# Kernel tuning notes

Measured on AMD Instinct MI355X. Metric: run time of the kernel, lower is better.

The kernel has to match this reference:

```python
import jax, jax.numpy as jnp
import numpy as np

N_EXPERTS = 16
TOP_K = 4
N_GROUP = 4
TOPK_GROUP = 2
NORM_TOPK = True
ROUTED_SCALE = 2.5
H = 2048
F_MOE = 1024
F_SHARED = 2048
B, S = 2, 2048


def setup_inputs() -> dict:
    key = jax.random.key(0)
    ks = jax.random.split(key, 9)
    std = 0.02
    return {
        "hidden_states": jax.random.normal(ks[0], (B, S, H), jnp.float32),
        "gate_weight": jax.random.normal(ks[1], (N_EXPERTS, H), jnp.float32) * std,
        "e_score_correction_bias": jnp.zeros((N_EXPERTS,), jnp.float32),
        "gate_w": jax.random.normal(ks[2], (N_EXPERTS, F_MOE, H), jnp.float32) * std,
        "up_w": jax.random.normal(ks[3], (N_EXPERTS, F_MOE, H), jnp.float32) * std,
        "down_w": jax.random.normal(ks[4], (N_EXPERTS, H, F_MOE), jnp.float32) * std,
        "sh_gate_w": jax.random.normal(ks[5], (F_SHARED, H), jnp.float32) * std,
        "sh_up_w": jax.random.normal(ks[6], (F_SHARED, H), jnp.float32) * std,
        "sh_down_w": jax.random.normal(ks[7], (H, F_SHARED), jnp.float32) * std,
    }


def _route(hidden, gate_weight, bias):
    # hidden: [T, H] -> topk_weight [T, K], topk_idx [T, K]
    T = hidden.shape[0]
    epg = N_EXPERTS // N_GROUP
    logits = hidden @ gate_weight.T                     # [T, N]
    scores = jax.nn.sigmoid(logits)
    scores_for_choice = scores + bias[None, :]
    # group score = sum of top-2 per group
    grp = scores_for_choice.reshape(T, N_GROUP, epg)
    group_scores = jax.lax.top_k(grp, 2)[0].sum(-1)      # [T, G]
    group_idx = jax.lax.top_k(group_scores, TOPK_GROUP)[1]
    group_mask = jax.nn.one_hot(group_idx, N_GROUP, dtype=jnp.bool_).any(1)  # [T, G]
    score_mask = jnp.repeat(group_mask, epg, axis=-1)    # [T, N]
    masked = jnp.where(score_mask, scores_for_choice, -jnp.inf)
    topk_idx = jax.lax.top_k(masked, TOP_K)[1]           # [T, K]
    topk_weight = jnp.take_along_axis(scores, topk_idx, axis=1)  # raw sigmoid scores
    return topk_weight, topk_idx


def _swiglu(x, gw, uw, dw):
    return (jax.nn.silu(x @ gw.T) * (x @ uw.T)) @ dw.T


def reference(hidden_states, gate_weight, e_score_correction_bias,
              gate_w, up_w, down_w, sh_gate_w, sh_up_w, sh_down_w):
    Bh, Sh, Hh = hidden_states.shape
    hidden = hidden_states.reshape(-1, Hh)               # [T, H]
    topk_weight, topk_idx = _route(hidden, gate_weight, e_score_correction_bias)
    if NORM_TOPK:
        topk_weight = topk_weight / (topk_weight.sum(-1, keepdims=True) + 1e-20)
    topk_weight = topk_weight * ROUTED_SCALE
    # dense dispatch weight matrix [T, N] (sum of one-hot * weight over k)
    one_hot = jax.nn.one_hot(topk_idx, N_EXPERTS, dtype=topk_weight.dtype)
    weight_matrix = (one_hot * topk_weight[..., None]).sum(1)
    # run all experts densely (faithful to original)
    g = jnp.einsum('th,nfh->ntf', hidden, gate_w)        # [N, T, F]
    u = jnp.einsum('th,nfh->ntf', hidden, up_w)
    act = jax.nn.silu(g) * u
    routed = jnp.einsum('ntf,nhf,tn->th', act, down_w, weight_matrix)
    out = routed + _swiglu(hidden, sh_gate_w, sh_up_w, sh_down_w)
    return out.reshape(Bh, Sh, Hh)
```

## Files before the change

### kernel.cpp

```cpp
#include <hip/hip_runtime.h>
#include <cstdint>

typedef unsigned int u32;
typedef unsigned short u16;
typedef __bf16 bf16x8 __attribute__((ext_vector_type(8)));
typedef float f32x4 __attribute__((ext_vector_type(4)));

#define NTOK 4096
#define HDIM 2048
#define FMOE 1024
#define FSH  2048
#define NEXP 16

__device__ __forceinline__ u16 f2bf(float f) {
  u32 u = __float_as_uint(f);
  u32 r = (u + 0x7fffu + ((u >> 16) & 1u)) >> 16;
  return (u16)r;
}
__device__ __forceinline__ float bf2f(u16 h) {
  return __uint_as_float(((u32)h) << 16);
}

__device__ __forceinline__ void gld_lds16(const void* g, void* l) {
  __builtin_amdgcn_global_load_lds(
      (const __attribute__((address_space(1))) u32*)g,
      (__attribute__((address_space(3))) u32*)l, 16, 0, 0);
}

__global__ void cvt_bf16(const float* __restrict__ in, u16* __restrict__ out, long n4) {
  long i = (long)blockIdx.x * blockDim.x + threadIdx.x;
  if (i < n4) {
    float4 v = ((const float4*)in)[i];
    ushort4 o;
    o.x = f2bf(v.x); o.y = f2bf(v.y); o.z = f2bf(v.z); o.w = f2bf(v.w);
    ((ushort4*)out)[i] = o;
  }
}

__global__ void cvt_pair_moe(const float* __restrict__ g, const float* __restrict__ u,
                             u16* __restrict__ dst) {
  int e = blockIdx.z;
  const long n4 = (long)FMOE * HDIM / 4;
  long i = (long)blockIdx.x * blockDim.x + threadIdx.x;
  const float4* gs = (const float4*)(g + (long)e * FMOE * HDIM);
  const float4* us = (const float4*)(u + (long)e * FMOE * HDIM);
  ushort4* d = (ushort4*)(dst + (long)e * 2 * FMOE * HDIM);
  float4 v = gs[i];
  ushort4 o;
  o.x = f2bf(v.x); o.y = f2bf(v.y); o.z = f2bf(v.z); o.w = f2bf(v.w);
  d[i] = o;
  v = us[i];
  o.x = f2bf(v.x); o.y = f2bf(v.y); o.z = f2bf(v.z); o.w = f2bf(v.w);
  d[n4 + i] = o;
}

__global__ __launch_bounds__(256) void routing_kernel(
    const float* __restrict__ hidden, const float* __restrict__ gw,
    const float* __restrict__ bias, int* __restrict__ topk_idx,
    float* __restrict__ topk_w) {
  __shared__ float gws[8 * HDIM];
  int tid = threadIdx.x, lane = tid & 63, wv = tid >> 6;
  int t = blockIdx.x * 4 + wv;
  float acc[NEXP];
#pragma unroll
  for (int n = 0; n < NEXP; ++n) acc[n] = 0.f;
  const float4* h4 = (const float4*)(hidden + (long)t * HDIM);

  for (int half = 0; half < 2; ++half) {
    for (int i = tid; i < 8 * HDIM / 4; i += 256)
      ((float4*)gws)[i] = ((const float4*)(gw + half * 8 * HDIM))[i];
    __syncthreads();
#pragma unroll
    for (int j0 = 0; j0 < HDIM / 4; j0 += 64) {
      int j = j0 + lane;
      float4 hv = h4[j];
#pragma unroll
      for (int e = 0; e < 8; ++e) {
        float4 g = ((const float4*)gws)[e * (HDIM / 4) + j];
        acc[half * 8 + e] += hv.x * g.x + hv.y * g.y + hv.z * g.z + hv.w * g.w;
      }
    }
    __syncthreads();
  }
#pragma unroll
  for (int n = 0; n < NEXP; ++n) {
    float v = acc[n];
    for (int m = 32; m; m >>= 1) v += __shfl_xor(v, m);
    acc[n] = v;
  }
  if (lane == 0) {
    float sc[NEXP], scb[NEXP];
#pragma unroll
    for (int n = 0; n < NEXP; ++n) {
      sc[n] = 1.f / (1.f + expf(-acc[n]));
      scb[n] = sc[n] + bias[n];
    }
    float gs[4];
#pragma unroll
    for (int g = 0; g < 4; ++g) {
      float m1 = -1e30f, m2 = -1e30f;
#pragma unroll
      for (int j = 0; j < 4; ++j) {
        float v = scb[4 * g + j];
        if (v > m1) { m2 = m1; m1 = v; } else if (v > m2) { m2 = v; }
      }
      gs[g] = m1 + m2;
    }
    int g1 = -1, g2 = -1;
    { float b = -1e30f; for (int g = 0; g < 4; ++g) if (gs[g] > b) { b = gs[g]; g1 = g; } }
    { float b = -1e30f; for (int g = 0; g < 4; ++g) if (g != g1 && gs[g] > b) { b = gs[g]; g2 = g; } }
    bool used[NEXP];
#pragma unroll
    for (int n = 0; n < NEXP; ++n) used[n] = false;
    int sel[4]; float wts[4]; float s = 0.f;
    for (int k = 0; k < 4; ++k) {
      float b = -1e30f; int bi = 0;
      for (int n = 0; n < NEXP; ++n) {
        int g = n >> 2;
        if ((g == g1 || g == g2) && !used[n] && scb[n] > b) { b = scb[n]; bi = n; }
      }
      used[bi] = true; sel[k] = bi; wts[k] = sc[bi]; s += sc[bi];
    }
    float inv = 2.5f / (s + 1e-20f);
    for (int k = 0; k < 4; ++k) {
      topk_idx[t * 4 + k] = sel[k];
      topk_w[t * 4 + k] = wts[k] * inv;
    }
  }
}

__global__ __launch_bounds__(256) void count_prefix(const int* __restrict__ topki,
                                                    int* __restrict__ offs) {
  __shared__ int wsum[4][NEXP];
  int tid = threadIdx.x, lane = tid & 63, wv = tid >> 6;
  int c[NEXP];
#pragma unroll
  for (int e = 0; e < NEXP; ++e) c[e] = 0;
  for (int i0 = wv * 64; i0 < NTOK * 4; i0 += 256) {
    int v = topki[i0 + lane];
#pragma unroll
    for (int e = 0; e < NEXP; ++e) {
      unsigned long long b = __ballot(v == e);
      if (lane == 0) c[e] += __popcll(b);
    }
  }
  if (lane == 0) {
#pragma unroll
    for (int e = 0; e < NEXP; ++e) wsum[wv][e] = c[e];
  }
  __syncthreads();
  if (tid == 0) {
    int s = 0;
    for (int e = 0; e < NEXP; ++e) {
      int t = wsum[0][e] + wsum[1][e] + wsum[2][e] + wsum[3][e];
      offs[e] = s;
      s += t;
    }
    offs[NEXP] = s;
  }
}

__global__ void fill_lists(const int* __restrict__ topk_idx,
                           const int* __restrict__ offs, int* __restrict__ ltok,
                           int* __restrict__ slotmap) {
  int e = blockIdx.x;
  int tid = threadIdx.x, lane = tid & 63, wv = tid >> 6;
  __shared__ int cursor;
  __shared__ int wcnt[4];
  if (tid == 0) cursor = offs[e];
  __syncthreads();
  for (int base = 0; base < NTOK; base += 256) {
    int t = base + tid;
    int flag = 0, kk = 0;
#pragma unroll
    for (int k = 0; k < 4; ++k) {
      if (topk_idx[t * 4 + k] == e) { flag = 1; kk = k; }
    }
    unsigned long long b = __ballot(flag);
    if (lane == 0) wcnt[wv] = __popcll(b);
    __syncthreads();
    int pre = 0;
    for (int i = 0; i < wv; ++i) pre += wcnt[i];
    int pos = cursor + pre + __popcll(b & ((1ull << lane) - 1ull));
    if (flag) { ltok[pos] = t; slotmap[t * 4 + kk] = pos; }
    __syncthreads();
    if (tid == 0) cursor += wcnt[0] + wcnt[1] + wcnt[2] + wcnt[3];
    __syncthreads();
  }
}

template <int F>
__global__ void silu_mul_pair(u16* __restrict__ gu, const int* __restrict__ nrows_ptr,
                              int nrows_static) {
  int rows = nrows_ptr ? *nrows_ptr : nrows_static;
  long total4 = (long)rows * (F / 4);
  long i = (long)blockIdx.x * blockDim.x + threadIdx.x;
  if (i < total4) {
    long row = i / (F / 4);
    int f4 = (int)(i - row * (F / 4));
    ushort4* rowp = (ushort4*)(gu + row * 2 * F);
    ushort4 gv = rowp[f4];
    ushort4 uv = rowp[F / 4 + f4];
    float gf, uf, sv;
    ushort4 o;
    gf = bf2f(gv.x); uf = bf2f(uv.x); sv = gf / (1.f + __expf(-gf)); o.x = f2bf(sv * uf);
    gf = bf2f(gv.y); uf = bf2f(uv.y); sv = gf / (1.f + __expf(-gf)); o.y = f2bf(sv * uf);
    gf = bf2f(gv.z); uf = bf2f(uv.z); sv = gf / (1.f + __expf(-gf)); o.z = f2bf(sv * uf);
    gf = bf2f(gv.w); uf = bf2f(uv.w); sv = gf / (1.f + __expf(-gf)); o.w = f2bf(sv * uf);
    rowp[f4] = o;
  }
}

__global__ void reduce_out(const u16* __restrict__ SY, const u16* __restrict__ Y,
                           const int* __restrict__ slotmap, const float* __restrict__ tkw,
                           float* __restrict__ out) {
  long i = (long)blockIdx.x * blockDim.x + threadIdx.x;
  int t = (int)(i >> 9);
  int c4 = (int)(i & 511);
  ushort4 s = ((const ushort4*)SY)[i];
  float4 o;
  o.x = bf2f(s.x); o.y = bf2f(s.y); o.z = bf2f(s.z); o.w = bf2f(s.w);
#pragma unroll
  for (int k = 0; k < 4; ++k) {
    int sl = slotmap[t * 4 + k];
    float w = tkw[t * 4 + k];
    ushort4 y = ((const ushort4*)Y)[(long)sl * 512 + c4];
    o.x += w * bf2f(y.x);
    o.y += w * bf2f(y.y);
    o.z += w * bf2f(y.z);
    o.w += w * bf2f(y.w);
  }
  ((float4*)out)[i] = o;
}

#define LGKM0 asm volatile("s_waitcnt lgkmcnt(0)" ::: "memory")
#define VMC4  asm volatile("s_waitcnt vmcnt(4)" ::: "memory")
#define VMC0  asm volatile("s_waitcnt vmcnt(0)" ::: "memory")
__device__ __forceinline__ void bar() {
  asm volatile("" ::: "memory");
  __builtin_amdgcn_s_barrier();
  asm volatile("" ::: "memory");
}

__global__ __launch_bounds__(512, 2) void gemm256(
    const u16* __restrict__ A, const u16* __restrict__ B, u16* __restrict__ C,
    const int* __restrict__ gather, const int* __restrict__ offs,
    int Mstatic, int N, int K, int lda, long Bstride) {
  int e = blockIdx.z;
  int seg0 = 0, segM = Mstatic;
  if (offs) { seg0 = offs[e]; segM = offs[e + 1] - seg0; }
  int mt = blockIdx.y, nt = blockIdx.x;
  if (mt * 256 >= segM) return;
  const u16* Be = B + (long)e * Bstride;

  __shared__ __align__(16) u16 sm[65536];

  int tid = threadIdx.x;
  int lane = tid & 63;
  int wv = tid >> 6, wm = wv >> 2, wn = wv & 3;
  int c4 = lane & 15, r4 = lane >> 4;

  int srow = tid >> 3, schunk = tid & 7;
  int sswz8 = (schunk ^ (srow & 7)) * 8;
  int sOff = srow * 64 + schunk * 8;

  u32 aoff[2][2], boff[2][2];
#pragma unroll
  for (int h = 0; h < 2; ++h)
#pragma unroll
    for (int j = 0; j < 2; ++j) {
      int rit = h * 128 + j * 64 + srow;
      int rl = mt * 256 + rit;
      if (rl >= segM) rl = mt * 256;
      int ridx = seg0 + rl;
      u32 arow = gather ? (u32)gather[ridx] : (u32)ridx;
      aoff[h][j] = arow * (u32)lda + (u32)sswz8;
      boff[h][j] = (u32)(nt * 256 + rit) * (u32)K + (u32)sswz8;
    }

  int swzv = (lane & 7) * 8;
  int aRL0 = c4 * 64 + ((r4 * 8) ^ swzv);
  int aRL1 = aRL0 ^ 32;
  int aB0 = wm * 8192, aB1 = 32768 + aB0;
  int bB0 = 16384 + wn * 4096, bB1 = 32768 + bB0;

  f32x4 acc[8][4];
  bf16x8 af[4][2], bLo[2][2], bHi[2][2];
#pragma unroll
  for (int i = 0; i < 8; ++i)
#pragma unroll
    for (int j = 0; j < 4; ++j) acc[i][j] = f32x4{0.f, 0.f, 0.f, 0.f};

#define READ_A8(BASE) do { _Pragma("unroll") \
  for (int mi = 0; mi < 4; ++mi) { \
    af[mi][0] = *(const bf16x8*)&sm[(BASE) + mi * 1024 + aRL0]; \
    af[mi][1] = *(const bf16x8*)&sm[(BASE) + mi * 1024 + aRL1]; \
  } } while (0)
#define READ_B4(BASE, BARR) do { _Pragma("unroll") \
  for (int ni = 0; ni < 2; ++ni) { \
    BARR[ni][0] = *(const bf16x8*)&sm[(BASE) + ni * 1024 + aRL0]; \
    BARR[ni][1] = *(const bf16x8*)&sm[(BASE) + ni * 1024 + aRL1]; \
  } } while (0)
#define MFMAQ(MI0, NI0, BARR) do { __builtin_amdgcn_s_setprio(1); \
  _Pragma("unroll") for (int mi = 0; mi < 4; ++mi) \
  _Pragma("unroll") for (int ni = 0; ni < 2; ++ni) \
  _Pragma("unroll") for (int kk = 0; kk < 2; ++kk) \
    acc[(MI0) + mi][(NI0) + ni] = __builtin_amdgcn_mfma_f32_16x16x32_bf16( \
        af[mi][kk], BARR[ni][kk], acc[(MI0) + mi][(NI0) + ni], 0, 0, 0); \
  __builtin_amdgcn_s_setprio(0); } while (0)
#define STAGE_A(PO, H, T) do { \
  gld_lds16(A + aoff[H][0] + (u32)((T) * 64), &sm[(PO) + (H) * 8192 + sOff]); \
  gld_lds16(A + aoff[H][1] + (u32)((T) * 64), &sm[(PO) + (H) * 8192 + 4096 + sOff]); \
} while (0)
#define STAGE_B(PO, H, T) do { \
  gld_lds16(Be + boff[H][0] + (u32)((T) * 64), &sm[(PO) + 16384 + (H) * 8192 + sOff]); \
  gld_lds16(Be + boff[H][1] + (u32)((T) * 64), &sm[(PO) + 16384 + (H) * 8192 + 4096 + sOff]); \
} while (0)

  STAGE_A(0, 0, 0); STAGE_A(0, 1, 0); STAGE_B(0, 0, 0); STAGE_B(0, 1, 0);
  STAGE_B(32768, 0, 1); STAGE_B(32768, 1, 1);
  VMC4;
  bar();

  int niter = K >> 7;
  for (int it = 0; it < niter; ++it) {
    int to = 2 * it + 1, t2 = 2 * it + 2, t3 = 2 * it + 3;
    bool nl = (it + 1 < niter);
    READ_A8(aB0); READ_B4(bB0, bLo);
    STAGE_A(32768, 0, to);
    bar(); LGKM0; MFMAQ(0, 0, bLo); bar();
    READ_B4(bB0 + 2048, bHi);
    STAGE_A(32768, 1, to);
    bar(); LGKM0; MFMAQ(0, 2, bHi); bar();
    READ_A8(aB0 + 4096);
    if (nl) STAGE_B(0, 0, t2);
    bar(); LGKM0; MFMAQ(4, 2, bHi); bar();
    if (nl) { STAGE_B(0, 1, t2); VMC4; } else { VMC0; }
    bar(); MFMAQ(4, 0, bLo); bar();
    READ_A8(aB1); READ_B4(bB1, bLo);
    if (nl) STAGE_A(0, 0, t2);
    bar(); LGKM0; MFMAQ(0, 0, bLo); bar();
    READ_B4(bB1 + 2048, bHi);
    if (nl) STAGE_A(0, 1, t2);
    bar(); LGKM0; MFMAQ(0, 2, bHi); bar();
    READ_A8(aB1 + 4096);
    if (nl) STAGE_B(32768, 0, t3);
    bar(); LGKM0; MFMAQ(4, 2, bHi); bar();
    if (nl) { STAGE_B(32768, 1, t3); VMC4; }
    bar(); MFMAQ(4, 0, bLo); bar();
  }

#undef READ_A8
#undef READ_B4
#undef MFMAQ
#undef STAGE_A
#undef STAGE_B

#pragma unroll
  for (int mi = 0; mi < 8; ++mi) {
#pragma unroll
    for (int r = 0; r < 4; ++r) {
      int lr = wm * 128 + mi * 16 + r4 * 4 + r;
      if (mt * 256 + lr < segM) {
        long base = (long)(seg0 + mt * 256 + lr) * N + nt * 256 + wn * 64 + c4;
#pragma unroll
        for (int ni = 0; ni < 4; ++ni) C[base + ni * 16] = f2bf(acc[mi][ni][r]);
      }
    }
  }
}

extern "C" void kernel_launch(void* const* d_in, const int* in_sizes, int n_in,
                              void* d_out, int out_size, void* d_ws, size_t ws_size,
                              hipStream_t stream) {
  const float* hidden = (const float*)d_in[0];
  const float* gate_weight = (const float*)d_in[1];
  const float* bias = (const float*)d_in[2];
  const float* gate_w = (const float*)d_in[3];
  const float* up_w = (const float*)d_in[4];
  const float* down_w = (const float*)d_in[5];
  const float* shg = (const float*)d_in[6];
  const float* shu = (const float*)d_in[7];
  const float* shd = (const float*)d_in[8];
  float* out = (float*)d_out;

  char* p = (char*)d_ws;
  auto alloc = [&](size_t bytes) {
    char* q = p;
    p += (bytes + 255) & ~(size_t)255;
    return q;
  };
  u16* Xb = (u16*)alloc((size_t)NTOK * HDIM * 2);
  u16* GUb = (u16*)alloc((size_t)NEXP * 2 * FMOE * HDIM * 2);
  u16* Db = (u16*)alloc((size_t)NEXP * HDIM * FMOE * 2);
  u16* SGUb = (u16*)alloc((size_t)2 * FSH * HDIM * 2);
  u16* SDb = (u16*)alloc((size_t)HDIM * FSH * 2);
  u16* gu_out = (u16*)alloc((size_t)NTOK * 4 * 2 * FMOE * 2);
  int* topki = (int*)alloc((size_t)NTOK * 4 * 4);
  float* topkw = (float*)alloc((size_t)NTOK * 4 * 4);
  int* offs = (int*)alloc(128);
  int* ltok = (int*)alloc((size_t)NTOK * 4 * 4);
  int* slotmap = (int*)alloc((size_t)NTOK * 4 * 4);
  u16* Y = GUb;
  u16* gs_out = GUb + (size_t)NTOK * 4 * HDIM;
  u16* SY = gs_out + (size_t)NTOK * 2 * FSH;

  cvt_bf16<<<8192, 256, 0, stream>>>(hidden, Xb, (long)NTOK * HDIM / 4);
  cvt_pair_moe<<<dim3(2048, 1, NEXP), 256, 0, stream>>>(gate_w, up_w, GUb);
  cvt_bf16<<<32768, 256, 0, stream>>>(down_w, Db, (long)NEXP * HDIM * FMOE / 4);
  cvt_bf16<<<4096, 256, 0, stream>>>(shg, SGUb, (long)FSH * HDIM / 4);
  cvt_bf16<<<4096, 256, 0, stream>>>(shu, SGUb + (size_t)FSH * HDIM, (long)FSH * HDIM / 4);
  cvt_bf16<<<4096, 256, 0, stream>>>(shd, SDb, (long)HDIM * FSH / 4);

  routing_kernel<<<NTOK / 4, 256, 0, stream>>>(hidden, gate_weight, bias, topki, topkw);
  count_prefix<<<1, 256, 0, stream>>>(topki, offs);
  fill_lists<<<NEXP, 256, 0, stream>>>(topki, offs, ltok, slotmap);

  gemm256<<<dim3(2 * FMOE / 256, NTOK / 256, NEXP), 512, 0, stream>>>(
      Xb, GUb, gu_out, ltok, offs, 0, 2 * FMOE, HDIM, HDIM, (long)2 * FMOE * HDIM);
  silu_mul_pair<FMOE><<<16384, 256, 0, stream>>>(gu_out, offs + NEXP, 0);
  gemm256<<<dim3(HDIM / 256, NTOK / 256, NEXP), 512, 0, stream>>>(
      gu_out, Db, Y, nullptr, offs, 0, HDIM, FMOE, 2 * FMOE, (long)HDIM * FMOE);

  gemm256<<<dim3(2 * FSH / 256, NTOK / 256, 1), 512, 0, stream>>>(
      Xb, SGUb, gs_out, nullptr, nullptr, NTOK, 2 * FSH, HDIM, HDIM, 0);
  silu_mul_pair<FSH><<<8192, 256, 0, stream>>>(gs_out, nullptr, NTOK);
  gemm256<<<dim3(HDIM / 256, NTOK / 256, 1), 512, 0, stream>>>(
      gs_out, SDb, SY, nullptr, nullptr, NTOK, HDIM, FSH, 2 * FSH, 0);

  reduce_out<<<8192, 256, 0, stream>>>(SY, Y, slotmap, topkw, out);
}
```

Before: 962.8 us.

## Fuse SiLU-mul into gate/up GEMM epilogue via interleaved weight layout

Weights for gate and up projections are reordered during conversion so that each 256-column GEMM tile holds 128 gate and 128 up columns. The GEMM epilogue then exchanges the up half through shared memory and writes silu(g)*u directly, which removes the separate silu_mul kernels and halves the intermediate buffer written and read by the down GEMM. Separately, the routing kernel drops the LDS staging of gate weights and reads them directly from global/cache with the hidden row held in registers. This costs extra LDS traffic and barriers in the epilogue, plus strided scatter writes in the conversion kernel.

```diff
diff --git a/kernel.cpp b/kernel.cpp
--- a/kernel.cpp
+++ b/kernel.cpp
@@ -37,50 +37,50 @@
   }
 }
 
-__global__ void cvt_pair_moe(const float* __restrict__ g, const float* __restrict__ u,
-                             u16* __restrict__ dst) {
+template <int F>
+__global__ void cvt_pair(const float* __restrict__ g, const float* __restrict__ u,
+                         u16* __restrict__ dst) {
   int e = blockIdx.z;
-  const long n4 = (long)FMOE * HDIM / 4;
+  const long n4 = (long)F * HDIM / 4;
   long i = (long)blockIdx.x * blockDim.x + threadIdx.x;
-  const float4* gs = (const float4*)(g + (long)e * FMOE * HDIM);
-  const float4* us = (const float4*)(u + (long)e * FMOE * HDIM);
-  ushort4* d = (ushort4*)(dst + (long)e * 2 * FMOE * HDIM);
+  if (i >= n4) return;
+  int f = (int)(i >> 9);
+  int c = (int)(i & 511);
+  const float4* gs = (const float4*)(g + (long)e * F * HDIM);
+  const float4* us = (const float4*)(u + (long)e * F * HDIM);
+  ushort4* d = (ushort4*)(dst + (long)e * 2 * F * HDIM);
+  long rg = (long)(256 * (f >> 7) + (f & 127)) * 512 + c;
+  long ru = rg + 128 * 512;
   float4 v = gs[i];
   ushort4 o;
   o.x = f2bf(v.x); o.y = f2bf(v.y); o.z = f2bf(v.z); o.w = f2bf(v.w);
-  d[i] = o;
+  d[rg] = o;
   v = us[i];
   o.x = f2bf(v.x); o.y = f2bf(v.y); o.z = f2bf(v.z); o.w = f2bf(v.w);
-  d[n4 + i] = o;
+  d[ru] = o;
 }
 
 __global__ __launch_bounds__(256) void routing_kernel(
     const float* __restrict__ hidden, const float* __restrict__ gw,
     const float* __restrict__ bias, int* __restrict__ topk_idx,
     float* __restrict__ topk_w) {
-  __shared__ float gws[8 * HDIM];
   int tid = threadIdx.x, lane = tid & 63, wv = tid >> 6;
   int t = blockIdx.x * 4 + wv;
+  const float4* h4 = (const float4*)(hidden + (long)t * HDIM);
+  const float4* g4 = (const float4*)gw;
+  float4 hv[8];
+#pragma unroll
+  for (int j = 0; j < 8; ++j) hv[j] = h4[lane + 64 * j];
   float acc[NEXP];
 #pragma unroll
-  for (int n = 0; n < NEXP; ++n) acc[n] = 0.f;
-  const float4* h4 = (const float4*)(hidden + (long)t * HDIM);
-
-  for (int half = 0; half < 2; ++half) {
-    for (int i = tid; i < 8 * HDIM / 4; i += 256)
-      ((float4*)gws)[i] = ((const float4*)(gw + half * 8 * HDIM))[i];
-    __syncthreads();
-#pragma unroll
-    for (int j0 = 0; j0 < HDIM / 4; j0 += 64) {
-      int j = j0 + lane;
-      float4 hv = h4[j];
-#pragma unroll
-      for (int e = 0; e < 8; ++e) {
-        float4 g = ((const float4*)gws)[e * (HDIM / 4) + j];
-        acc[half * 8 + e] += hv.x * g.x + hv.y * g.y + hv.z * g.z + hv.w * g.w;
-      }
-    }
-    __syncthreads();
+  for (int e = 0; e < NEXP; ++e) {
+    float a = 0.f;
+#pragma unroll
+    for (int j = 0; j < 8; ++j) {
+      float4 g = g4[e * 512 + lane + 64 * j];
+      a += hv[j].x * g.x + hv[j].y * g.y + hv[j].z * g.z + hv[j].w * g.w;
+    }
+    acc[e] = a;
   }
 #pragma unroll
   for (int n = 0; n < NEXP; ++n) {
@@ -189,28 +189,6 @@
   }
 }
 
-template <int F>
-__global__ void silu_mul_pair(u16* __restrict__ gu, const int* __restrict__ nrows_ptr,
-                              int nrows_static) {
-  int rows = nrows_ptr ? *nrows_ptr : nrows_static;
-  long total4 = (long)rows * (F / 4);
-  long i = (long)blockIdx.x * blockDim.x + threadIdx.x;
-  if (i < total4) {
-    long row = i / (F / 4);
-    int f4 = (int)(i - row * (F / 4));
-    ushort4* rowp = (ushort4*)(gu + row * 2 * F);
-    ushort4 gv = rowp[f4];
-    ushort4 uv = rowp[F / 4 + f4];
-    float gf, uf, sv;
-    ushort4 o;
-    gf = bf2f(gv.x); uf = bf2f(uv.x); sv = gf / (1.f + __expf(-gf)); o.x = f2bf(sv * uf);
-    gf = bf2f(gv.y); uf = bf2f(uv.y); sv = gf / (1.f + __expf(-gf)); o.y = f2bf(sv * uf);
-    gf = bf2f(gv.z); uf = bf2f(uv.z); sv = gf / (1.f + __expf(-gf)); o.z = f2bf(sv * uf);
-    gf = bf2f(gv.w); uf = bf2f(uv.w); sv = gf / (1.f + __expf(-gf)); o.w = f2bf(sv * uf);
-    rowp[f4] = o;
-  }
-}
-
 __global__ void reduce_out(const u16* __restrict__ SY, const u16* __restrict__ Y,
                            const int* __restrict__ slotmap, const float* __restrict__ tkw,
                            float* __restrict__ out) {
@@ -245,7 +223,7 @@
 __global__ __launch_bounds__(512, 2) void gemm256(
     const u16* __restrict__ A, const u16* __restrict__ B, u16* __restrict__ C,
     const int* __restrict__ gather, const int* __restrict__ offs,
-    int Mstatic, int N, int K, int lda, long Bstride) {
+    int Mstatic, int N, int K, int lda, long Bstride, int fuse) {
   int e = blockIdx.z;
   int seg0 = 0, segM = Mstatic;
   if (offs) { seg0 = offs[e]; segM = offs[e + 1] - seg0; }
@@ -356,15 +334,85 @@
 #undef STAGE_A
 #undef STAGE_B
 
-#pragma unroll
-  for (int mi = 0; mi < 8; ++mi) {
-#pragma unroll
-    for (int r = 0; r < 4; ++r) {
-      int lr = wm * 128 + mi * 16 + r4 * 4 + r;
-      if (mt * 256 + lr < segM) {
-        long base = (long)(seg0 + mt * 256 + lr) * N + nt * 256 + wn * 64 + c4;
-#pragma unroll
-        for (int ni = 0; ni < 4; ++ni) C[base + ni * 16] = f2bf(acc[mi][ni][r]);
+  if (fuse) {
+    if (wn >= 2) {
+#pragma unroll
+      for (int mi = 0; mi < 4; ++mi)
+#pragma unroll
+        for (int ni = 0; ni < 4; ++ni)
+#pragma unroll
+          for (int r = 0; r < 4; ++r) {
+            int rloc = mi * 16 + r4 * 4 + r;
+            int floc = (wn - 2) * 64 + ni * 16 + c4;
+            sm[(wm * 128 + rloc) * 128 + floc] = f2bf(acc[mi + 4 * 0][ni][r]);
+          }
+    }
+    __syncthreads();
+    if (wn < 2) {
+#pragma unroll
+      for (int mi = 0; mi < 4; ++mi)
+#pragma unroll
+        for (int r = 0; r < 4; ++r) {
+          int rloc = mi * 16 + r4 * 4 + r;
+          int lr = wm * 128 + rloc;
+          if (mt * 256 + lr < segM) {
+            long base = (long)(seg0 + mt * 256 + lr) * (N >> 1) + nt * 128 + wn * 64 + c4;
+#pragma unroll
+            for (int ni = 0; ni < 4; ++ni) {
+              float g = acc[mi][ni][r];
+              float u = bf2f(sm[(wm * 128 + rloc) * 128 + wn * 64 + ni * 16 + c4]);
+              float a = g / (1.f + __expf(-g)) * u;
+              C[base + ni * 16] = f2bf(a);
+            }
+          }
+        }
+    }
+    if (wn >= 2) {
+    }
+    __syncthreads();
+    if (wn >= 2) {
+#pragma unroll
+      for (int mi = 0; mi < 4; ++mi)
+#pragma unroll
+        for (int ni = 0; ni < 4; ++ni)
+#pragma unroll
+          for (int r = 0; r < 4; ++r) {
+            int rloc = mi * 16 + r4 * 4 + r;
+            int floc = (wn - 2) * 64 + ni * 16 + c4;
+            sm[(wm * 128 + rloc) * 128 + floc] = f2bf(acc[mi + 4][ni][r]);
+          }
+    }
+    __syncthreads();
+    if (wn < 2) {
+#pragma unroll
+      for (int mi = 0; mi < 4; ++mi)
+#pragma unroll
+        for (int r = 0; r < 4; ++r) {
+          int rloc = mi * 16 + r4 * 4 + r;
+          int lr = wm * 128 + 64 + rloc;
+          if (mt * 256 + lr < segM) {
+            long base = (long)(seg0 + mt * 256 + lr) * (N >> 1) + nt * 128 + wn * 64 + c4;
+#pragma unroll
+            for (int ni = 0; ni < 4; ++ni) {
+              float g = acc[mi + 4][ni][r];
+              float u = bf2f(sm[(wm * 128 + rloc) * 128 + wn * 64 + ni * 16 + c4]);
+              float a = g / (1.f + __expf(-g)) * u;
+              C[base + ni * 16] = f2bf(a);
+            }
+          }
+        }
+    }
+  } else {
+#pragma unroll
+    for (int mi = 0; mi < 8; ++mi) {
+#pragma unroll
+      for (int r = 0; r < 4; ++r) {
+        int lr = wm * 128 + mi * 16 + r4 * 4 + r;
+        if (mt * 256 + lr < segM) {
+          long base = (long)(seg0 + mt * 256 + lr) * N + nt * 256 + wn * 64 + c4;
+#pragma unroll
+          for (int ni = 0; ni < 4; ++ni) C[base + ni * 16] = f2bf(acc[mi][ni][r]);
+        }
       }
     }
   }
@@ -395,7 +443,7 @@
   u16* Db = (u16*)alloc((size_t)NEXP * HDIM * FMOE * 2);
   u16* SGUb = (u16*)alloc((size_t)2 * FSH * HDIM * 2);
   u16* SDb = (u16*)alloc((size_t)HDIM * FSH * 2);
-  u16* gu_out = (u16*)alloc((size_t)NTOK * 4 * 2 * FMOE * 2);
+  u16* gu_out = (u16*)alloc((size_t)NTOK * 4 * FMOE * 2);
   int* topki = (int*)alloc((size_t)NTOK * 4 * 4);
   float* topkw = (float*)alloc((size_t)NTOK * 4 * 4);
   int* offs = (int*)alloc(128);
@@ -403,13 +451,12 @@
   int* slotmap = (int*)alloc((size_t)NTOK * 4 * 4);
   u16* Y = GUb;
   u16* gs_out = GUb + (size_t)NTOK * 4 * HDIM;
-  u16* SY = gs_out + (size_t)NTOK * 2 * FSH;
+  u16* SY = gs_out + (size_t)NTOK * FSH;
 
   cvt_bf16<<<8192, 256, 0, stream>>>(hidden, Xb, (long)NTOK * HDIM / 4);
-  cvt_pair_moe<<<dim3(2048, 1, NEXP), 256, 0, stream>>>(gate_w, up_w, GUb);
+  cvt_pair<FMOE><<<dim3(2048, 1, NEXP), 256, 0, stream>>>(gate_w, up_w, GUb);
   cvt_bf16<<<32768, 256, 0, stream>>>(down_w, Db, (long)NEXP * HDIM * FMOE / 4);
-  cvt_bf16<<<4096, 256, 0, stream>>>(shg, SGUb, (long)FSH * HDIM / 4);
-  cvt_bf16<<<4096, 256, 0, stream>>>(shu, SGUb + (size_t)FSH * HDIM, (long)FSH * HDIM / 4);
+  cvt_pair<FSH><<<dim3(4096, 1, 1), 256, 0, stream>>>(shg, shu, SGUb);
   cvt_bf16<<<4096, 256, 0, stream>>>(shd, SDb, (long)HDIM * FSH / 4);
 
   routing_kernel<<<NTOK / 4, 256, 0, stream>>>(hidden, gate_weight, bias, topki, topkw);
@@ -417,16 +464,14 @@
   fill_lists<<<NEXP, 256, 0, stream>>>(topki, offs, ltok, slotmap);
 
   gemm256<<<dim3(2 * FMOE / 256, NTOK / 256, NEXP), 512, 0, stream>>>(
-      Xb, GUb, gu_out, ltok, offs, 0, 2 * FMOE, HDIM, HDIM, (long)2 * FMOE * HDIM);
-  silu_mul_pair<FMOE><<<16384, 256, 0, stream>>>(gu_out, offs + NEXP, 0);
+      Xb, GUb, gu_out, ltok, offs, 0, 2 * FMOE, HDIM, HDIM, (long)2 * FMOE * HDIM, 1);
   gemm256<<<dim3(HDIM / 256, NTOK / 256, NEXP), 512, 0, stream>>>(
-      gu_out, Db, Y, nullptr, offs, 0, HDIM, FMOE, 2 * FMOE, (long)HDIM * FMOE);
+      gu_out, Db, Y, nullptr, offs, 0, HDIM, FMOE, FMOE, (long)HDIM * FMOE, 0);
 
   gemm256<<<dim3(2 * FSH / 256, NTOK / 256, 1), 512, 0, stream>>>(
-      Xb, SGUb, gs_out, nullptr, nullptr, NTOK, 2 * FSH, HDIM, HDIM, 0);
-  silu_mul_pair<FSH><<<8192, 256, 0, stream>>>(gs_out, nullptr, NTOK);
+      Xb, SGUb, gs_out, nullptr, nullptr, NTOK, 2 * FSH, HDIM, HDIM, 0, 1);
   gemm256<<<dim3(HDIM / 256, NTOK / 256, 1), 512, 0, stream>>>(
-      gs_out, SDb, SY, nullptr, nullptr, NTOK, HDIM, FSH, 2 * FSH, 0);
+      gs_out, SDb, SY, nullptr, nullptr, NTOK, HDIM, FSH, FSH, 0, 0);
 
   reduce_out<<<8192, 256, 0, stream>>>(SY, Y, slotmap, topkw, out);
 }
```

Result: no change. 981.9 us (+2.0%).
